# Performance work log

Measured on AMD Instinct MI355X. Metric: run time of the kernel, lower is better.

Reference implementation:

```python
import jax, jax.numpy as jnp
import numpy as np

P = 16      # patch size
DM = 512    # d_model
DI = 1024   # d_inner = expand * d_model
N = 16      # d_state
K = 4       # d_conv
DR = 32     # dt_rank = ceil(d_model/16)
NL = 8      # n_layers
NC = 1000   # num_classes


def _ln(x, w, b):
    m = x.mean(-1, keepdims=True)
    v = x.var(-1, keepdims=True)
    return (x - m) * jax.lax.rsqrt(v + 1e-5) * w + b


def _fpad(x, wl, wr, ht, hb):
    # torch F.pad(x, (wl, wr, ht, hb)) with possibly negative (crop) values, NCHW
    x = jnp.pad(x, ((0, 0), (0, 0), (max(ht, 0), max(hb, 0)), (max(wl, 0), max(wr, 0))))
    return x[:, :, -min(ht, 0):x.shape[2] + min(hb, 0), -min(wl, 0):x.shape[3] + min(wr, 0)]


def _mamba(x, in_w, conv_w, conv_b, xproj_w, dt_w, dt_b, A_log, Dp, out_w):
    # standard mamba_ssm Mamba layer; weights stored (in, out)
    B, L, _ = x.shape
    xz = x @ in_w                         # (B, L, 2*DI)
    xpart, z = xz[..., :DI], xz[..., DI:]
    # depthwise causal conv1d, kernel K, padding K-1 then truncate to L
    xc = jnp.pad(xpart.transpose(0, 2, 1), ((0, 0), (0, 0), (K - 1, 0)))  # (B, DI, L+K-1)
    conv = conv_b[None, :, None] + sum(conv_w[None, :, k, None] * xc[:, :, k:k + L] for k in range(K))
    u = jax.nn.silu(conv).transpose(0, 2, 1)    # (B, L, DI)
    dbc = u @ xproj_w                           # (B, L, DR + 2N)
    dt = jax.nn.softplus(dbc[..., :DR] @ dt_w + dt_b)  # (B, L, DI)
    Bm, Cm = dbc[..., DR:DR + N], dbc[..., DR + N:]
    A = -jnp.exp(A_log)                         # (DI, N)
    dA = jnp.exp(dt[..., None] * A)             # (B, L, DI, N)
    dBu = (dt * u)[..., None] * Bm[:, :, None, :]

    def step(h, inp):
        dA_t, dBu_t, C_t = inp
        h = dA_t * h + dBu_t                    # (B, DI, N)
        return h, jnp.einsum('bdn,bn->bd', h, C_t)

    h0 = jnp.zeros((B, DI, N), x.dtype)
    _, ys = jax.lax.scan(step, h0, (dA.transpose(1, 0, 2, 3), dBu.transpose(1, 0, 2, 3), Cm.transpose(1, 0, 2)))
    y = ys.transpose(1, 0, 2) + u * Dp          # (B, L, DI)
    return (y * jax.nn.silu(z)) @ out_w         # (B, L, DM)


def reference(img, patch_ln_w, patch_ln_b, patch_w, patch_b, pos_emb, cls_tok,
              ln_w, ln_b, in_w, conv_w, conv_b, xproj_w, dt_w, dt_b, A_log, D, out_w,
              head_ln_w, head_ln_b, head_w, head_b):
    shifts = ((1, -1, 0, 0), (-1, 1, 0, 0), (0, 0, 1, -1), (0, 0, -1, 1))
    x5 = jnp.concatenate([img] + [_fpad(img, *s) for s in shifts], axis=1)  # (B, 15, H, W)
    Bn, C, H, W = x5.shape
    # 'b c (h p1) (w p2) -> b (h w) (p1 p2 c)'
    x = x5.reshape(Bn, C, H // P, P, W // P, P).transpose(0, 2, 4, 3, 5, 1).reshape(Bn, (H // P) * (W // P), P * P * C)
    x = _ln(x, patch_ln_w, patch_ln_b) @ patch_w + patch_b  # (B, n, DM)
    n = x.shape[1]
    x = jnp.concatenate([x, jnp.broadcast_to(cls_tok, (Bn, 1, DM))], axis=1)  # cls appended at END
    x = x + pos_emb[:, :n + 1]
    for i in range(NL):
        y = _ln(x, ln_w[i], ln_b[i])
        x = x + _mamba(y, in_w[i], conv_w[i], conv_b[i], xproj_w[i], dt_w[i], dt_b[i], A_log[i], D[i], out_w[i])
    x = x[:, -1]  # pool='cls' -> last token
    return _ln(x, head_ln_w, head_ln_b) @ head_w + head_b


def setup_inputs() -> dict:
    key = jax.random.key(0)
    ks = jax.random.split(key, 12)
    B = 8
    PD = P * P * 15  # 3840
    rn = lambda k, shape, scale=1.0: jax.random.normal(k, shape, jnp.float32) * scale
    return {
        "img": rn(ks[0], (B, 3, 224, 224)),
        "patch_ln_w": jnp.ones((PD,), jnp.float32), "patch_ln_b": jnp.zeros((PD,), jnp.float32),
        "patch_w": rn(ks[1], (PD, DM), PD ** -0.5), "patch_b": jnp.zeros((DM,), jnp.float32),
        "pos_emb": rn(ks[2], (1, 197, DM), 0.02),
        "cls_tok": rn(ks[3], (1, 1, DM), 0.02),
        "ln_w": jnp.ones((NL, DM), jnp.float32), "ln_b": jnp.zeros((NL, DM), jnp.float32),
        "in_w": rn(ks[4], (NL, DM, 2 * DI), DM ** -0.5),
        "conv_w": rn(ks[5], (NL, DI, K), K ** -0.5),
        "conv_b": jnp.zeros((NL, DI), jnp.float32),
        "xproj_w": rn(ks[6], (NL, DI, DR + 2 * N), DI ** -0.5),
        "dt_w": rn(ks[7], (NL, DR, DI), DR ** -0.5),
        "dt_b": rn(ks[8], (NL, DI), 0.1) - 4.0,  # softplus -> small positive dt
        "A_log": jnp.log(jnp.broadcast_to(jnp.arange(1.0, N + 1.0, dtype=jnp.float32), (NL, DI, N))),
        "D": jnp.ones((NL, DI), jnp.float32),
        "out_w": rn(ks[9], (NL, DI, DM), DI ** -0.5),
        "head_ln_w": jnp.ones((DM,), jnp.float32), "head_ln_b": jnp.zeros((DM,), jnp.float32),
        "head_w": rn(ks[10], (DM, NC), DM ** -0.5), "head_b": jnp.zeros((NC,), jnp.float32),
    }
```

## Files before the change

kernel.cpp:

```cpp
#include <hip/hip_runtime.h>
#include <hip/hip_fp16.h>
#include <math.h>

#define BATCH   8
#define LSEQ    197
#define LPAD    200
#define NPATCH  196
#define NPTOK   (BATCH * NPATCH)
#define NTOK    (BATCH * LSEQ)
#define MPAD    1664
#define DMODEL  512
#define DINNER  1024
#define NSTATE  16
#define DRANK   32
#define NLAYER  8
#define NCLS    1000
#define PDIM    3840

typedef _Float16 f16x8 __attribute__((ext_vector_type(8)));
typedef float    f32x4 __attribute__((ext_vector_type(4)));
typedef unsigned short us8 __attribute__((ext_vector_type(8)));

__device__ __forceinline__ float f_rcp(float x) { return __builtin_amdgcn_rcpf(x); }
__device__ __forceinline__ float sp_silu(float x) { return x * f_rcp(1.0f + __expf(-x)); }
__device__ __forceinline__ float sp_softplus(float x) {
    return x > 20.0f ? x : __logf(1.0f + __expf(x));
}

template <int N>
__device__ __forceinline__ void vm_wait() {
    if constexpr (N == 0)       asm volatile("s_waitcnt vmcnt(0)" ::: "memory");
    else if constexpr (N == 4)  asm volatile("s_waitcnt vmcnt(4)" ::: "memory");
    else if constexpr (N == 6)  asm volatile("s_waitcnt vmcnt(6)" ::: "memory");
    else if constexpr (N == 8)  asm volatile("s_waitcnt vmcnt(8)" ::: "memory");
    else if constexpr (N == 12) asm volatile("s_waitcnt vmcnt(12)" ::: "memory");
}

#define DPP_ROW_SHR_STEP(P, NB, CTRL)                                          \
    {                                                                          \
        float t_[NB];                                                          \
        _Pragma("unroll")                                                      \
        for (int i_ = 0; i_ < NB; ++i_)                                        \
            t_[i_] = __int_as_float(__builtin_amdgcn_update_dpp(               \
                0, __float_as_int(P[i_]), CTRL, 0xF, 0xF, true));              \
        _Pragma("unroll")                                                      \
        for (int i_ = 0; i_ < NB; ++i_) P[i_] += t_[i_];                       \
    }

template <int NB>
__device__ __forceinline__ void row_sum16v(float* p) {
    DPP_ROW_SHR_STEP(p, NB, 0x111);
    DPP_ROW_SHR_STEP(p, NB, 0x112);
    DPP_ROW_SHR_STEP(p, NB, 0x114);
    DPP_ROW_SHR_STEP(p, NB, 0x118);
}

__device__ __forceinline__ void store_f16(char* __restrict__ Hb,
                                          int row, int k, int K, float v) {
    size_t byte = (size_t)row * (size_t)(K * 2) +
                  (size_t)(((unsigned)(k * 2)) ^ (unsigned)((row & 7) << 4));
    *(__half*)(Hb + byte) = __float2half_rn(v);
}

__device__ __forceinline__ void store_f16x4(char* __restrict__ Hb,
                                            int row, int k4, int K, float4 v) {
    size_t byte = (size_t)row * (size_t)(K * 2) +
                  (size_t)(((unsigned)(k4 * 2)) ^ (unsigned)((row & 7) << 4));
    *(ushort4*)(Hb + byte) = make_ushort4(
        __half_as_ushort(__float2half_rn(v.x)), __half_as_ushort(__float2half_rn(v.y)),
        __half_as_ushort(__float2half_rn(v.z)), __half_as_ushort(__float2half_rn(v.w)));
}

__device__ __forceinline__ float2 block_reduce2(float a, float b, float* lds) {
#pragma unroll
    for (int off = 32; off > 0; off >>= 1) {
        a += __shfl_down(a, off);
        b += __shfl_down(b, off);
    }
    int lane = threadIdx.x & 63, w = threadIdx.x >> 6;
    if (lane == 0) { lds[w] = a; lds[4 + w] = b; }
    __syncthreads();
    float sa = lds[0] + lds[1] + lds[2] + lds[3];
    float sb = lds[4] + lds[5] + lds[6] + lds[7];
    return make_float2(sa, sb);
}

__global__ __launch_bounds__(256) void k_patch_ln(
    const float* __restrict__ img, const float* __restrict__ lnw,
    const float* __restrict__ lnb, char* __restrict__ Xph) {
    __shared__ float vals[PDIM];
    __shared__ float red[8];
    int tok = blockIdx.x;
    int b = tok / NPATCH, p = tok % NPATCH;
    int gy = p / 14, gx = p % 14;
    int tid = threadIdx.x;
    int py = tid >> 4, px = tid & 15;
    int h0 = gy * 16 + py, w0 = gx * 16 + px;
    const int dh[5] = {0, 0, 0, -1, 1};
    const int dw[5] = {0, -1, 1, 0, 0};
    float s = 0.f, ss = 0.f;
#pragma unroll
    for (int c = 0; c < 15; ++c) {
        int g = c / 3, ch = c % 3;
        int h = h0 + dh[g], w = w0 + dw[g];
        float v = 0.f;
        if ((unsigned)h < 224u && (unsigned)w < 224u)
            v = img[((b * 3 + ch) * 224 + h) * 224 + w];
        vals[tid * 15 + c] = v;
        s += v; ss += v * v;
    }
    float2 t2 = block_reduce2(s, ss, red);
    float mean = t2.x * (1.0f / PDIM);
    float var  = t2.y * (1.0f / PDIM) - mean * mean;
    float rstd = 1.0f / sqrtf(var + 1e-5f);
    for (int j = 0; j < 15; ++j) {
        int e = tid + j * 256;
        float v = (vals[e] - mean) * rstd * lnw[e] + lnb[e];
        store_f16(Xph, tok, e, PDIM, v);
    }
}

__global__ __launch_bounds__(256) void k_ln(
    const float* __restrict__ x, const float* __restrict__ w,
    const float* __restrict__ b, char* __restrict__ yh) {
    __shared__ float red[8];
    int t = blockIdx.x, tid = threadIdx.x;
    const float* xr = x + (size_t)t * DMODEL;
    float v0 = xr[tid], v1 = xr[tid + 256];
    float2 t2 = block_reduce2(v0 + v1, v0 * v0 + v1 * v1, red);
    float mean = t2.x * (1.0f / DMODEL);
    float var  = t2.y * (1.0f / DMODEL) - mean * mean;
    float rstd = 1.0f / sqrtf(var + 1e-5f);
    store_f16(yh, t, tid,       DMODEL, (v0 - mean) * rstd * w[tid]       + b[tid]);
    store_f16(yh, t, tid + 256, DMODEL, (v1 - mean) * rstd * w[tid + 256] + b[tid + 256]);
}

__global__ __launch_bounds__(256) void k_red_ln(
    const float* __restrict__ part, float* __restrict__ xtok,
    const float* __restrict__ w, const float* __restrict__ b,
    char* __restrict__ yh) {
    __shared__ float red[8];
    int t = blockIdx.x, tid = threadIdx.x;
    size_t base = (size_t)t * DMODEL;
    float v0 = xtok[base + tid], v1 = xtok[base + tid + 256];
#pragma unroll
    for (int k = 0; k < 2; ++k) {
        v0 += part[(size_t)k * (NTOK * DMODEL) + base + tid];
        v1 += part[(size_t)k * (NTOK * DMODEL) + base + tid + 256];
    }
    xtok[base + tid] = v0;
    xtok[base + tid + 256] = v1;
    float2 t2 = block_reduce2(v0 + v1, v0 * v0 + v1 * v1, red);
    float mean = t2.x * (1.0f / DMODEL);
    float var  = t2.y * (1.0f / DMODEL) - mean * mean;
    float rstd = 1.0f / sqrtf(var + 1e-5f);
    store_f16(yh, t, tid,       DMODEL, (v0 - mean) * rstd * w[tid]       + b[tid]);
    store_f16(yh, t, tid + 256, DMODEL, (v1 - mean) * rstd * w[tid + 256] + b[tid + 256]);
}

__global__ __launch_bounds__(256) void k_wT(
    const float* __restrict__ W, char* __restrict__ Th,
    int Ks, int Ns, size_t wStride, size_t tByteStride) {
    __shared__ float t[32][33];
    int z = blockIdx.z;
    const float* Wz = W + (size_t)z * wStride;
    char* ThZ = Th + (size_t)z * tByteStride;
    int n0 = blockIdx.x * 32, k0 = blockIdx.y * 32;
    int tx = threadIdx.x, ty = threadIdx.y;
#pragma unroll
    for (int r = 0; r < 4; ++r) {
        int k = k0 + ty + r * 8, n = n0 + tx;
        t[tx][ty + r * 8] = (n < Ns) ? Wz[(size_t)k * Ns + n] : 0.f;
    }
    __syncthreads();
#pragma unroll
    for (int r = 0; r < 4; ++r) {
        int n = n0 + ty + r * 8, k = k0 + tx;
        float v = t[ty + r * 8][tx];
        size_t byte = (size_t)n * (size_t)(Ks * 2) +
                      (size_t)(((unsigned)(k * 2)) ^ (unsigned)((n & 7) << 4));
        *(__half*)(ThZ + byte) = __float2half_rn(v);
    }
}

template <int TM, int TN, bool F16OUT>
__global__ __launch_bounds__(256, 2) void k_gemm(
    const char* __restrict__ Ah, const char* __restrict__ Bh,
    float* __restrict__ C, unsigned short* __restrict__ C16,
    int M, int N, int K, int kchunk, long partStride) {
    constexpr int MW = TM / 2, NW = TN / 2;
    constexpr int FM = MW / 16, FN = NW / 16;
    constexpr int CPW = (TM + TN) / 32;
    __shared__ __half L[3][(TM + TN) * 64];
    const int tid = threadIdx.x, w = tid >> 6, lane = tid & 63;

    const int GX = gridDim.x, GY = gridDim.y;
    const int nwg = GX * GY * gridDim.z;
    const int orig = blockIdx.x + GX * (blockIdx.y + GY * blockIdx.z);
    const int q = nwg >> 3, r = nwg & 7, xcd = orig & 7, pos = orig >> 3;
    const int wrk = (xcd < r ? xcd * (q + 1) : r * (q + 1) + (xcd - r) * q) + pos;
    const int bm = wrk % GY;
    const int t1 = wrk / GY;
    const int bn = t1 % GX, bz = t1 / GX;

    const int m0 = bm * TM, n0 = bn * TN;
    const int kbeg = bz * kchunk;
    int kend = kbeg + kchunk; if (kend > K) kend = K;
    C += (size_t)bz * (size_t)partStride;
    const size_t K2 = (size_t)K * 2;
    const int srLane = lane >> 3;
    const int scol = (lane & 7) * 16;

    f32x4 acc[FM][FN];
#pragma unroll
    for (int i = 0; i < FM; ++i)
#pragma unroll
        for (int j = 0; j < FN; ++j) acc[i][j] = (f32x4)(0.f);

    auto STAGE = [&](int buf, int k0) {
#pragma unroll
        for (int i = 0; i < CPW; ++i) {
            int cid = w * CPW + i;
            bool isA = cid < TM / 8;
            int lr = (isA ? cid : cid - TM / 8) * 8;
            size_t go = (size_t)((isA ? m0 : n0) + lr + srLane) * K2 +
                        (size_t)k0 * 2 + scol;
            const char* src = isA ? Ah : Bh;
            int ldsOff = (isA ? 0 : TM * 64) + lr * 64;
            __builtin_amdgcn_global_load_lds(
                (const __attribute__((address_space(1))) void*)(src + go),
                (__attribute__((address_space(3))) void*)&L[buf][ldsOff], 16, 0, 0);
        }
    };

    const int wm = w >> 1, wn = w & 1;
    const int g = lane >> 4, rr = lane & 15;
    const int nk = (kend - kbeg + 63) / 64;

    STAGE(0, kbeg);
    if (1 < nk) STAGE(1, kbeg + 64);

    for (int t = 0; t < nk; ++t) {
        if (t + 2 < nk) {
            STAGE((t + 2) % 3, kbeg + (t + 2) * 64);
            vm_wait<2 * CPW>();
        } else if (t + 1 < nk) {
            vm_wait<CPW>();
        } else {
            vm_wait<0>();
        }
        __builtin_amdgcn_s_barrier();
        const char* Lb = (const char*)L[t % 3];
#pragma unroll
        for (int kk = 0; kk < 2; ++kk) {
            f16x8 af[FM], bf[FN];
#pragma unroll
            for (int mf = 0; mf < FM; ++mf) {
                int row = wm * MW + mf * 16 + rr;
                int off = row * 128 + ((kk * 64 + g * 16) ^ ((row & 7) << 4));
                af[mf] = *(const f16x8*)(Lb + off);
            }
#pragma unroll
            for (int nf = 0; nf < FN; ++nf) {
                int row = wn * NW + nf * 16 + rr;
                int off = TM * 128 + row * 128 +
                          ((kk * 64 + g * 16) ^ ((row & 7) << 4));
                bf[nf] = *(const f16x8*)(Lb + off);
            }
#pragma unroll
            for (int mf = 0; mf < FM; ++mf)
#pragma unroll
                for (int nf = 0; nf < FN; ++nf)
                    acc[mf][nf] = __builtin_amdgcn_mfma_f32_16x16x32_f16(
                        af[mf], bf[nf], acc[mf][nf], 0, 0, 0);
        }
        __builtin_amdgcn_s_barrier();
    }

#pragma unroll
    for (int mf = 0; mf < FM; ++mf)
#pragma unroll
        for (int nf = 0; nf < FN; ++nf)
#pragma unroll
            for (int e = 0; e < 4; ++e) {
                int gm = m0 + wm * MW + mf * 16 + g * 4 + e;
                int gn = n0 + wn * NW + nf * 16 + rr;
                if (gm < M && gn < N) {
                    if (F16OUT)
                        C16[(size_t)gm * N + gn] =
                            __half_as_ushort(__float2half_rn(acc[mf][nf][e]));
                    else
                        C[(size_t)gm * N + gn] = acc[mf][nf][e];
                }
            }
}

template <int SK, bool ACC>
__global__ __launch_bounds__(256) void k_reduce(
    const float* __restrict__ part, float* __restrict__ out, int total, int stride) {
    int i = blockIdx.x * 256 + threadIdx.x;
    if (i >= total) return;
    float s = 0.f;
#pragma unroll
    for (int k = 0; k < SK; ++k) s += part[(size_t)k * stride + i];
    out[i] = ACC ? out[i] + s : s;
}

__global__ __launch_bounds__(256) void k_patch_asm(
    const float* __restrict__ part, const float* __restrict__ patch_b,
    const float* __restrict__ cls, const float* __restrict__ pos,
    float* __restrict__ xtok) {
    int idx = blockIdx.x * 256 + threadIdx.x;
    if (idx >= NTOK * DMODEL) return;
    int d = idx % DMODEL;
    int t = (idx / DMODEL) % LSEQ;
    int b = idx / (DMODEL * LSEQ);
    float v;
    if (t < NPATCH) {
        size_t pi = ((size_t)(b * NPATCH + t)) * DMODEL + d;
        float s = patch_b[d];
#pragma unroll
        for (int k = 0; k < 4; ++k) s += part[(size_t)k * (NPTOK * DMODEL) + pi];
        v = s;
    } else {
        v = cls[d];
    }
    xtok[idx] = v + pos[t * DMODEL + d];
}

__global__ __launch_bounds__(256) void k_conv(
    const unsigned short* __restrict__ xzH, const float* __restrict__ cw,
    const float* __restrict__ cb, char* __restrict__ uh) {
    int idx = blockIdx.x * 256 + threadIdx.x;
    if (idx >= NTOK * (DINNER / 4)) return;
    int dq = idx & (DINNER / 4 - 1);
    int t  = idx / (DINNER / 4);
    int l  = t % LSEQ;
    int d  = dq * 4;
    float4 w0 = *(const float4*)&cw[(d + 0) * 4];
    float4 w1 = *(const float4*)&cw[(d + 1) * 4];
    float4 w2 = *(const float4*)&cw[(d + 2) * 4];
    float4 w3 = *(const float4*)&cw[(d + 3) * 4];
    float4 acc = *(const float4*)&cb[d];
#pragma unroll
    for (int j = 0; j < 4; ++j) {
        int ls = l - 3 + j;
        if (ls >= 0) {
            union { ushort4 v; __half h[4]; } xu;
            xu.v = *(const ushort4*)&xzH[(size_t)(t - 3 + j) * (2 * DINNER) + d];
            acc.x += (&w0.x)[j] * __half2float(xu.h[0]);
            acc.y += (&w1.x)[j] * __half2float(xu.h[1]);
            acc.z += (&w2.x)[j] * __half2float(xu.h[2]);
            acc.w += (&w3.x)[j] * __half2float(xu.h[3]);
        }
    }
    float4 uv = make_float4(sp_silu(acc.x), sp_silu(acc.y),
                            sp_silu(acc.z), sp_silu(acc.w));
    store_f16x4(uh, t, d, DINNER, uv);
}

__global__ __launch_bounds__(256) void k_scan2(
    const char* __restrict__ uH, const float* __restrict__ dbc,
    const float* __restrict__ dtw, const float* __restrict__ dtb,
    const float* __restrict__ Alog, const float* __restrict__ Dp,
    const unsigned short* __restrict__ xzH, char* __restrict__ gh) {
    __shared__ float uS[LPAD * 16];
    __shared__ float dS[LPAD * 16];
    __shared__ float bS[LPAD * 16];
    __shared__ float cS[LPAD * 16];
    __shared__ float wS[DRANK * 16];
    const int tid = threadIdx.x;
    const int b = blockIdx.y, d0 = blockIdx.x * 16;

    for (int i = tid; i < DRANK * 16; i += 256)
        wS[i] = dtw[(size_t)(i >> 4) * DINNER + d0 + (i & 15)];
    __syncthreads();

    for (int i = tid; i < LPAD * 2; i += 256) {
        int l = i >> 1, jj = i & 1;
        float* dst = &uS[l * 16 + jj * 8];
        if (l >= LSEQ) {
#pragma unroll
            for (int e = 0; e < 8; ++e) dst[e] = 0.f;
            continue;
        }
        int t = b * LSEQ + l;
        size_t byte = (size_t)t * (DINNER * 2) +
                      (size_t)(((unsigned)(d0 * 2 + jj * 16)) ^ (unsigned)((t & 7) << 4));
        union { us8 v; __half h[8]; } uu;
        uu.v = *(const us8*)(uH + byte);
#pragma unroll
        for (int e = 0; e < 8; ++e) dst[e] = __half2float(uu.h[e]);
    }

    const float* dbcB = dbc + ((size_t)b * LSEQ) * 64;
    for (int i = tid; i < LPAD * 4; i += 256) {
        int l = i >> 2, j = (i & 3) << 2;
        if (l >= LSEQ) {
            float4 z = make_float4(0.f, 0.f, 0.f, 0.f);
            *(float4*)&dS[l * 16 + j] = z;
            *(float4*)&bS[l * 16 + j] = z;
            *(float4*)&cS[l * 16 + j] = z;
            continue;
        }
        *(float4*)&bS[l * 16 + j] = *(const float4*)&dbcB[(size_t)l * 64 + DRANK + j];
        *(float4*)&cS[l * 16 + j] = *(const float4*)&dbcB[(size_t)l * 64 + DRANK + 16 + j];
        float4 acc = *(const float4*)&dtb[d0 + j];
#pragma unroll
        for (int kq = 0; kq < DRANK / 4; ++kq) {
            float4 r4 = *(const float4*)&dbcB[(size_t)l * 64 + kq * 4];
#pragma unroll
            for (int m = 0; m < 4; ++m) {
                float rv = (&r4.x)[m];
                float4 w4 = *(const float4*)&wS[(kq * 4 + m) * 16 + j];
                acc.x += rv * w4.x; acc.y += rv * w4.y;
                acc.z += rv * w4.z; acc.w += rv * w4.w;
            }
        }
        dS[l * 16 + j + 0] = sp_softplus(acc.x);
        dS[l * 16 + j + 1] = sp_softplus(acc.y);
        dS[l * 16 + j + 2] = sp_softplus(acc.z);
        dS[l * 16 + j + 3] = sp_softplus(acc.w);
    }
    const int n = tid & 15, dsub = tid >> 4;
    const int d = d0 + dsub;
    const float A  = -__expf(Alog[d * NSTATE + n]);
    const float Dv = Dp[d];

    ushort4 zreg[4];
#pragma unroll
    for (int it = 0; it < 4; ++it) {
        int i = tid + it * 256;
        if (i < LSEQ * 4) {
            int l = i >> 2, j = (i & 3) << 2;
            int t = b * LSEQ + l;
            zreg[it] = *(const ushort4*)&xzH[(size_t)t * (2 * DINNER) + DINNER + d0 + j];
        }
    }
    __syncthreads();

    float hn = 0.f;
    float dtc[8], uvc[8], Bnc[8], Cnc[8];
#pragma unroll
    for (int i = 0; i < 8; ++i) {
        int o = i * 16;
        dtc[i] = dS[o + dsub]; uvc[i] = uS[o + dsub];
        Bnc[i] = bS[o + n];    Cnc[i] = cS[o + n];
    }
    for (int lb = 0; lb < LPAD; lb += 8) {
        float dtN[8], uvN[8], BnN[8], CnN[8];
        if (lb + 8 < LPAD) {
#pragma unroll
            for (int i = 0; i < 8; ++i) {
                int o = (lb + 8 + i) * 16;
                dtN[i] = dS[o + dsub]; uvN[i] = uS[o + dsub];
                BnN[i] = bS[o + n];    CnN[i] = cS[o + n];
            }
        } else {
#pragma unroll
            for (int i = 0; i < 8; ++i) { dtN[i] = uvN[i] = BnN[i] = CnN[i] = 0.f; }
        }
        float a8[8], b8[8], p8[8];
#pragma unroll
        for (int i = 0; i < 8; ++i) {
            a8[i] = __expf(dtc[i] * A);
            b8[i] = dtc[i] * uvc[i] * Bnc[i];
        }
#pragma unroll
        for (int i = 0; i < 8; ++i) {
            hn = a8[i] * hn + b8[i];
            p8[i] = hn * Cnc[i];
        }
        row_sum16v<8>(p8);
#pragma unroll
        for (int i = 0; i < 8; ++i)
            if (n == 15) dS[(lb + i) * 16 + dsub] = p8[i] + uvc[i] * Dv;
#pragma unroll
        for (int i = 0; i < 8; ++i) {
            dtc[i] = dtN[i]; uvc[i] = uvN[i]; Bnc[i] = BnN[i]; Cnc[i] = CnN[i];
        }
    }
    __syncthreads();

#pragma unroll
    for (int it = 0; it < 4; ++it) {
        int i = tid + it * 256;
        if (i < LSEQ * 4) {
            int l = i >> 2, j = (i & 3) << 2;
            int t = b * LSEQ + l;
            union { ushort4 v; __half h[4]; } zu;
            zu.v = zreg[it];
            float4 g4 = make_float4(
                dS[l * 16 + j + 0] * sp_silu(__half2float(zu.h[0])),
                dS[l * 16 + j + 1] * sp_silu(__half2float(zu.h[1])),
                dS[l * 16 + j + 2] * sp_silu(__half2float(zu.h[2])),
                dS[l * 16 + j + 3] * sp_silu(__half2float(zu.h[3])));
            store_f16x4(gh, t, d0 + j, DINNER, g4);
        }
    }
}

__global__ __launch_bounds__(256) void k_head_ln(
    const float* __restrict__ part, const float* __restrict__ xtok,
    const float* __restrict__ lnw, const float* __restrict__ lnb,
    float* __restrict__ xr) {
    __shared__ float red[8];
    int b = blockIdx.x, tid = threadIdx.x;
    size_t base = ((size_t)(b * LSEQ + NPATCH)) * DMODEL;
    float v0 = xtok[base + tid], v1 = xtok[base + tid + 256];
#pragma unroll
    for (int k = 0; k < 2; ++k) {
        v0 += part[(size_t)k * (NTOK * DMODEL) + base + tid];
        v1 += part[(size_t)k * (NTOK * DMODEL) + base + tid + 256];
    }
    float2 t2 = block_reduce2(v0 + v1, v0 * v0 + v1 * v1, red);
    float mean = t2.x * (1.0f / DMODEL);
    float var  = t2.y * (1.0f / DMODEL) - mean * mean;
    float rstd = 1.0f / sqrtf(var + 1e-5f);
    xr[b * DMODEL + tid]       = (v0 - mean) * rstd * lnw[tid] + lnb[tid];
    xr[b * DMODEL + tid + 256] = (v1 - mean) * rstd * lnw[tid + 256] + lnb[tid + 256];
}

__global__ __launch_bounds__(256) void k_head_fc(
    const float* __restrict__ xr, const float* __restrict__ hw,
    float* __restrict__ hpart) {
    __shared__ float xs[64];
    int tid = threadIdx.x;
    int c = blockIdx.x * 256 + tid;
    int b = blockIdx.y, ks = blockIdx.z;
    if (tid < 64) xs[tid] = xr[b * DMODEL + ks * 64 + tid];
    __syncthreads();
    if (c >= NCLS) return;
    float acc = 0.f;
#pragma unroll 8
    for (int k = 0; k < 64; ++k) acc += xs[k] * hw[(size_t)(ks * 64 + k) * NCLS + c];
    hpart[(size_t)(ks * BATCH + b) * NCLS + c] = acc;
}

__global__ __launch_bounds__(256) void k_head_red(
    const float* __restrict__ hpart, const float* __restrict__ hb,
    float* __restrict__ out) {
    int i = blockIdx.x * 256 + threadIdx.x;
    if (i >= BATCH * NCLS) return;
    int b = i / NCLS, c = i % NCLS;
    float s = hb[c];
#pragma unroll
    for (int ks = 0; ks < 8; ++ks) s += hpart[(size_t)(ks * BATCH + b) * NCLS + c];
    out[i] = s;
}

extern "C" void kernel_launch(void* const* d_in, const int* in_sizes, int n_in,
                              void* d_out, int out_size, void* d_ws, size_t ws_size,
                              hipStream_t stream) {
    const float* img     = (const float*)d_in[0];
    const float* plnw    = (const float*)d_in[1];
    const float* plnb    = (const float*)d_in[2];
    const float* patch_w = (const float*)d_in[3];
    const float* patch_b = (const float*)d_in[4];
    const float* pos     = (const float*)d_in[5];
    const float* cls     = (const float*)d_in[6];
    const float* ln_w    = (const float*)d_in[7];
    const float* ln_b    = (const float*)d_in[8];
    const float* in_w    = (const float*)d_in[9];
    const float* conv_w  = (const float*)d_in[10];
    const float* conv_b  = (const float*)d_in[11];
    const float* xproj   = (const float*)d_in[12];
    const float* dt_w    = (const float*)d_in[13];
    const float* dt_b    = (const float*)d_in[14];
    const float* A_log   = (const float*)d_in[15];
    const float* Dp      = (const float*)d_in[16];
    const float* out_w   = (const float*)d_in[17];
    const float* hlnw    = (const float*)d_in[18];
    const float* hlnb    = (const float*)d_in[19];
    const float* head_w  = (const float*)d_in[20];
    const float* head_b  = (const float*)d_in[21];
    float* out = (float*)d_out;

    char* p = (char*)d_ws;
    auto alloc = [&](size_t bytes) { char* r = p; p += (bytes + 255) & ~(size_t)255; return r; };
    float* xtok = (float*)alloc((size_t)NTOK * DMODEL * 4);
    unsigned short* xzH = (unsigned short*)alloc((size_t)NTOK * 2 * DINNER * 2);
    float* dbc  = (float*)alloc((size_t)NTOK * 64 * 4);
    float* part = (float*)alloc((size_t)4 * NTOK * DMODEL * 4);
    float* xr   = (float*)alloc((size_t)BATCH * DMODEL * 4);
    float* hpart= (float*)alloc((size_t)8 * BATCH * NCLS * 4);
    char* ylnH = alloc((size_t)MPAD * DMODEL * 2);
    char* uH   = alloc((size_t)MPAD * DINNER * 2);
    char* gH   = alloc((size_t)MPAD * DINNER * 2);
    char* XpH  = alloc((size_t)MPAD * PDIM * 2);
    char* inTH  = alloc((size_t)NLAYER * 2 * DINNER * DMODEL * 2);
    char* outTH = alloc((size_t)NLAYER * DMODEL * DINNER * 2);
    char* patTH = alloc((size_t)DMODEL * PDIM * 2);
    char* xprTH = alloc((size_t)NLAYER * 128 * DINNER * 2);

    const size_t IN_T_B  = (size_t)2 * DINNER * DMODEL * 2;
    const size_t OUT_T_B = (size_t)DMODEL * DINNER * 2;
    const size_t XPR_T_B = (size_t)128 * DINNER * 2;

    k_wT<<<dim3(2 * DINNER / 32, DMODEL / 32, NLAYER), dim3(32, 8), 0, stream>>>(
        in_w, inTH, DMODEL, 2 * DINNER, (size_t)DMODEL * 2 * DINNER, IN_T_B);
    k_wT<<<dim3(DMODEL / 32, DINNER / 32, NLAYER), dim3(32, 8), 0, stream>>>(
        out_w, outTH, DINNER, DMODEL, (size_t)DINNER * DMODEL, OUT_T_B);
    k_wT<<<dim3(DMODEL / 32, PDIM / 32, 1), dim3(32, 8), 0, stream>>>(
        patch_w, patTH, PDIM, DMODEL, 0, 0);
    k_wT<<<dim3(128 / 32, DINNER / 32, NLAYER), dim3(32, 8), 0, stream>>>(
        xproj, xprTH, DINNER, 64, (size_t)DINNER * 64, XPR_T_B);

    k_patch_ln<<<NPTOK, 256, 0, stream>>>(img, plnw, plnb, XpH);
    k_gemm<64, 128, false><<<dim3(4, 25, 4), 256, 0, stream>>>(
        XpH, patTH, part, nullptr, NPTOK, DMODEL, PDIM, 960, (long)NPTOK * DMODEL);
    k_patch_asm<<<(NTOK * DMODEL + 255) / 256, 256, 0, stream>>>(
        part, patch_b, cls, pos, xtok);

    for (int i = 0; i < NLAYER; ++i) {
        if (i == 0) {
            k_ln<<<NTOK, 256, 0, stream>>>(xtok, ln_w, ln_b, ylnH);
        } else {
            k_red_ln<<<NTOK, 256, 0, stream>>>(part, xtok, ln_w + i * DMODEL,
                                               ln_b + i * DMODEL, ylnH);
        }
        k_gemm<64, 128, true><<<dim3(16, 25, 1), 256, 0, stream>>>(
            ylnH, inTH + i * IN_T_B, nullptr, xzH, NTOK, 2 * DINNER, DMODEL, DMODEL, 0);
        k_conv<<<(NTOK * (DINNER / 4) + 255) / 256, 256, 0, stream>>>(
            xzH, conv_w + (size_t)i * DINNER * 4, conv_b + (size_t)i * DINNER, uH);
        k_gemm<64, 64, false><<<dim3(1, 25, 4), 256, 0, stream>>>(
            uH, xprTH + i * XPR_T_B, part, nullptr, NTOK, 64, DINNER, 256, (long)NTOK * 64);
        k_reduce<4, false><<<(NTOK * 64 + 255) / 256, 256, 0, stream>>>(
            part, dbc, NTOK * 64, NTOK * 64);
        k_scan2<<<dim3(DINNER / 16, BATCH), 256, 0, stream>>>(
            uH, dbc, dt_w + (size_t)i * DRANK * DINNER, dt_b + (size_t)i * DINNER,
            A_log + (size_t)i * DINNER * NSTATE, Dp + (size_t)i * DINNER,
            xzH, gH);
        k_gemm<64, 128, false><<<dim3(4, 25, 2), 256, 0, stream>>>(
            gH, outTH + i * OUT_T_B, part, nullptr, NTOK, DMODEL, DINNER, 512,
            (long)NTOK * DMODEL);
    }

    k_head_ln<<<BATCH, 256, 0, stream>>>(part, xtok, hlnw, hlnb, xr);
    k_head_fc<<<dim3(4, BATCH, 8), 256, 0, stream>>>(xr, head_w, hpart);
    k_head_red<<<(BATCH * NCLS + 255) / 256, 256, 0, stream>>>(hpart, head_b, out);
}
```

Baseline: 545.6 us.

## Use wave-per-token layernorm, drop x_proj split-K reduce, rebalance patch split-K

The layernorm kernels now process one token per wavefront with shuffle-only reductions, so each block covers four tokens and the LDS barrier is gone. The x_proj GEMM writes directly to dbc without split-K, which removes the separate reduce kernel and one launch per layer, though only 25 blocks stay active. The patch-embedding GEMM moves from 4 to 6 split-K slices, with the assembly kernel summing 6 partials. The part buffer is resized to hold 6 patch partials.

```diff
diff --git a/kernel.cpp b/kernel.cpp
--- a/kernel.cpp
+++ b/kernel.cpp
@@ -85,6 +85,15 @@
     return make_float2(sa, sb);
 }
 
+__device__ __forceinline__ float2 wave_reduce2(float a, float b) {
+#pragma unroll
+    for (int off = 32; off > 0; off >>= 1) {
+        a += __shfl_xor(a, off);
+        b += __shfl_xor(b, off);
+    }
+    return make_float2(a, b);
+}
+
 __global__ __launch_bounds__(256) void k_patch_ln(
     const float* __restrict__ img, const float* __restrict__ lnw,
     const float* __restrict__ lnb, char* __restrict__ Xph) {
@@ -123,39 +132,58 @@
 __global__ __launch_bounds__(256) void k_ln(
     const float* __restrict__ x, const float* __restrict__ w,
     const float* __restrict__ b, char* __restrict__ yh) {
-    __shared__ float red[8];
-    int t = blockIdx.x, tid = threadIdx.x;
+    int wv = threadIdx.x >> 6, lane = threadIdx.x & 63;
+    int t = blockIdx.x * 4 + wv;
+    if (t >= NTOK) return;
     const float* xr = x + (size_t)t * DMODEL;
-    float v0 = xr[tid], v1 = xr[tid + 256];
-    float2 t2 = block_reduce2(v0 + v1, v0 * v0 + v1 * v1, red);
+    float v[8];
+    float s = 0.f, ss = 0.f;
+#pragma unroll
+    for (int j = 0; j < 8; ++j) {
+        v[j] = xr[lane + j * 64];
+        s += v[j]; ss += v[j] * v[j];
+    }
+    float2 t2 = wave_reduce2(s, ss);
     float mean = t2.x * (1.0f / DMODEL);
     float var  = t2.y * (1.0f / DMODEL) - mean * mean;
     float rstd = 1.0f / sqrtf(var + 1e-5f);
-    store_f16(yh, t, tid,       DMODEL, (v0 - mean) * rstd * w[tid]       + b[tid]);
-    store_f16(yh, t, tid + 256, DMODEL, (v1 - mean) * rstd * w[tid + 256] + b[tid + 256]);
+#pragma unroll
+    for (int j = 0; j < 8; ++j) {
+        int e = lane + j * 64;
+        store_f16(yh, t, e, DMODEL, (v[j] - mean) * rstd * w[e] + b[e]);
+    }
 }
 
 __global__ __launch_bounds__(256) void k_red_ln(
     const float* __restrict__ part, float* __restrict__ xtok,
     const float* __restrict__ w, const float* __restrict__ b,
     char* __restrict__ yh) {
-    __shared__ float red[8];
-    int t = blockIdx.x, tid = threadIdx.x;
+    int wv = threadIdx.x >> 6, lane = threadIdx.x & 63;
+    int t = blockIdx.x * 4 + wv;
+    if (t >= NTOK) return;
     size_t base = (size_t)t * DMODEL;
-    float v0 = xtok[base + tid], v1 = xtok[base + tid + 256];
-#pragma unroll
-    for (int k = 0; k < 2; ++k) {
-        v0 += part[(size_t)k * (NTOK * DMODEL) + base + tid];
-        v1 += part[(size_t)k * (NTOK * DMODEL) + base + tid + 256];
-    }
-    xtok[base + tid] = v0;
-    xtok[base + tid + 256] = v1;
-    float2 t2 = block_reduce2(v0 + v1, v0 * v0 + v1 * v1, red);
+    float v[8];
+    float s = 0.f, ss = 0.f;
+#pragma unroll
+    for (int j = 0; j < 8; ++j) {
+        int e = lane + j * 64;
+        float vv = xtok[base + e];
+#pragma unroll
+        for (int k = 0; k < 2; ++k)
+            vv += part[(size_t)k * (NTOK * DMODEL) + base + e];
+        xtok[base + e] = vv;
+        v[j] = vv;
+        s += vv; ss += vv * vv;
+    }
+    float2 t2 = wave_reduce2(s, ss);
     float mean = t2.x * (1.0f / DMODEL);
     float var  = t2.y * (1.0f / DMODEL) - mean * mean;
     float rstd = 1.0f / sqrtf(var + 1e-5f);
-    store_f16(yh, t, tid,       DMODEL, (v0 - mean) * rstd * w[tid]       + b[tid]);
-    store_f16(yh, t, tid + 256, DMODEL, (v1 - mean) * rstd * w[tid + 256] + b[tid + 256]);
+#pragma unroll
+    for (int j = 0; j < 8; ++j) {
+        int e = lane + j * 64;
+        store_f16(yh, t, e, DMODEL, (v[j] - mean) * rstd * w[e] + b[e]);
+    }
 }
 
 __global__ __launch_bounds__(256) void k_wT(
@@ -293,17 +321,6 @@
                         C[(size_t)gm * N + gn] = acc[mf][nf][e];
                 }
             }
-}
-
-template <int SK, bool ACC>
-__global__ __launch_bounds__(256) void k_reduce(
-    const float* __restrict__ part, float* __restrict__ out, int total, int stride) {
-    int i = blockIdx.x * 256 + threadIdx.x;
-    if (i >= total) return;
-    float s = 0.f;
-#pragma unroll
-    for (int k = 0; k < SK; ++k) s += part[(size_t)k * stride + i];
-    out[i] = ACC ? out[i] + s : s;
 }
 
 __global__ __launch_bounds__(256) void k_patch_asm(
@@ -320,7 +337,7 @@
         size_t pi = ((size_t)(b * NPATCH + t)) * DMODEL + d;
         float s = patch_b[d];
 #pragma unroll
-        for (int k = 0; k < 4; ++k) s += part[(size_t)k * (NPTOK * DMODEL) + pi];
+        for (int k = 0; k < 6; ++k) s += part[(size_t)k * (NPTOK * DMODEL) + pi];
         v = s;
     } else {
         v = cls[d];
@@ -581,7 +598,7 @@
     float* xtok = (float*)alloc((size_t)NTOK * DMODEL * 4);
     unsigned short* xzH = (unsigned short*)alloc((size_t)NTOK * 2 * DINNER * 2);
     float* dbc  = (float*)alloc((size_t)NTOK * 64 * 4);
-    float* part = (float*)alloc((size_t)4 * NTOK * DMODEL * 4);
+    float* part = (float*)alloc((size_t)6 * NPTOK * DMODEL * 4);
     float* xr   = (float*)alloc((size_t)BATCH * DMODEL * 4);
     float* hpart= (float*)alloc((size_t)8 * BATCH * NCLS * 4);
     char* ylnH = alloc((size_t)MPAD * DMODEL * 2);
@@ -607,26 +624,24 @@
         xproj, xprTH, DINNER, 64, (size_t)DINNER * 64, XPR_T_B);
 
     k_patch_ln<<<NPTOK, 256, 0, stream>>>(img, plnw, plnb, XpH);
-    k_gemm<64, 128, false><<<dim3(4, 25, 4), 256, 0, stream>>>(
-        XpH, patTH, part, nullptr, NPTOK, DMODEL, PDIM, 960, (long)NPTOK * DMODEL);
+    k_gemm<64, 128, false><<<dim3(4, 25, 6), 256, 0, stream>>>(
+        XpH, patTH, part, nullptr, NPTOK, DMODEL, PDIM, 640, (long)NPTOK * DMODEL);
     k_patch_asm<<<(NTOK * DMODEL + 255) / 256, 256, 0, stream>>>(
         part, patch_b, cls, pos, xtok);
 
     for (int i = 0; i < NLAYER; ++i) {
         if (i == 0) {
-            k_ln<<<NTOK, 256, 0, stream>>>(xtok, ln_w, ln_b, ylnH);
+            k_ln<<<(NTOK + 3) / 4, 256, 0, stream>>>(xtok, ln_w, ln_b, ylnH);
         } else {
-            k_red_ln<<<NTOK, 256, 0, stream>>>(part, xtok, ln_w + i * DMODEL,
-                                               ln_b + i * DMODEL, ylnH);
+            k_red_ln<<<(NTOK + 3) / 4, 256, 0, stream>>>(
+                part, xtok, ln_w + i * DMODEL, ln_b + i * DMODEL, ylnH);
         }
         k_gemm<64, 128, true><<<dim3(16, 25, 1), 256, 0, stream>>>(
             ylnH, inTH + i * IN_T_B, nullptr, xzH, NTOK, 2 * DINNER, DMODEL, DMODEL, 0);
         k_conv<<<(NTOK * (DINNER / 4) + 255) / 256, 256, 0, stream>>>(
             xzH, conv_w + (size_t)i * DINNER * 4, conv_b + (size_t)i * DINNER, uH);
-        k_gemm<64, 64, false><<<dim3(1, 25, 4), 256, 0, stream>>>(
-            uH, xprTH + i * XPR_T_B, part, nullptr, NTOK, 64, DINNER, 256, (long)NTOK * 64);
-        k_reduce<4, false><<<(NTOK * 64 + 255) / 256, 256, 0, stream>>>(
-            part, dbc, NTOK * 64, NTOK * 64);
+        k_gemm<64, 64, false><<<dim3(1, 25, 1), 256, 0, stream>>>(
+            uH, xprTH + i * XPR_T_B, dbc, nullptr, NTOK, 64, DINNER, DINNER, 0);
         k_scan2<<<dim3(DINNER / 16, BATCH), 256, 0, stream>>>(
             uH, dbc, dt_w + (size_t)i * DRANK * DINNER, dt_b + (size_t)i * DINNER,
             A_log + (size_t)i * DINNER * NSTATE, Dp + (size_t)i * DINNER,
```

New measurement: 562.5 us. +3.1%, slower.
